# Performance work log

Hardware: AMD Instinct MI355X
Metric: run time of the kernel (lower is better)

Reference implementation:

```python
import jax, jax.numpy as jnp
import numpy as np

B, V, SX, SY, TIN = 4, 3, 256, 256, 10
WIDTH, M1, M2, STEP, VOUT, NL = 32, 16, 16, 10, 3, 6


def setup_inputs() -> dict:
    key = jax.random.key(0)
    ks = jax.random.split(key, 20)
    n = lambda k, s, sc=1.0: sc * jax.random.normal(k, s, dtype=jnp.float32)
    u = lambda k, s: jax.random.uniform(k, s, dtype=jnp.float32)
    sc = 1.0 / WIDTH
    cshape = (NL, WIDTH, WIDTH, V, M1, M2)
    return {
        'x': n(ks[0], (B, V, SX, SY, TIN)),
        'fc0_w': n(ks[1], (TIN + 2, WIDTH), 0.1), 'fc0_b': jnp.zeros((WIDTH,), jnp.float32),
        'w1r': sc * u(ks[2], cshape), 'w1i': sc * u(ks[3], cshape),
        'w2r': sc * u(ks[4], cshape), 'w2i': sc * u(ks[5], cshape),
        'm1w': n(ks[6], (NL, WIDTH, WIDTH), 0.05), 'm1b': jnp.zeros((NL, WIDTH), jnp.float32),
        'm2w': n(ks[7], (NL, WIDTH, WIDTH), 0.05), 'm2b': jnp.zeros((NL, WIDTH), jnp.float32),
        'ww': n(ks[8], (NL, WIDTH, WIDTH), 0.05), 'wb': jnp.zeros((NL, WIDTH), jnp.float32),
        'bw': n(ks[9], (NL, WIDTH, 2), 0.1), 'bb': jnp.zeros((NL, WIDTH), jnp.float32),
        'fc1v_w': n(ks[10], (V, VOUT), 0.3), 'fc1v_b': jnp.zeros((VOUT,), jnp.float32),
        'fc1t_w': n(ks[11], (WIDTH, 256), 0.05), 'fc1t_b': jnp.zeros((256,), jnp.float32),
        'fc2t_w': n(ks[12], (256, STEP), 0.05), 'fc2t_b': jnp.zeros((STEP,), jnp.float32),
    }


def _gelu(t):
    return jax.nn.gelu(t, approximate=False)  # torch F.gelu default = exact erf


def _conv1x1(x, w, b):
    # 1x1x1 Conv3d: channel mix only. x: (b,c,v,x,y), w: (out,in)
    return jnp.einsum('bcvxy,oc->bovxy', x, w) + b[None, :, None, None, None]


def _spectral(x, w1, w2):
    # x: (b,c,v,X,Y); rfft2 over (X,Y); mode-truncated complex mix, zero-pad, irfft2
    sx, sy = x.shape[-2], x.shape[-1]
    xf = jnp.fft.rfft2(x)  # (b,c,v,X,Y//2+1) complex64
    o1 = jnp.einsum('bivxy,iovxy->bovxy', xf[..., :M1, :M2], w1)
    o2 = jnp.einsum('bivxy,iovxy->bovxy', xf[..., -M1:, :M2], w2)
    out = jnp.zeros((x.shape[0], w1.shape[1]) + xf.shape[2:], jnp.complex64)
    out = out.at[..., :M1, :M2].set(o1).at[..., -M1:, :M2].set(o2)
    return jnp.fft.irfft2(out, s=(sx, sy))


def reference(x, fc0_w, fc0_b, w1r, w1i, w2r, w2i, m1w, m1b, m2w, m2b, ww, wb, bw, bb,
              fc1v_w, fc1v_b, fc1t_w, fc1t_b, fc2t_w, fc2t_b):
    b, v, sx, sy, _ = x.shape
    gx = jnp.broadcast_to(jnp.linspace(0.0, 1.0, sx, dtype=jnp.float32)[:, None], (sx, sy))
    gy = jnp.broadcast_to(jnp.linspace(0.0, 1.0, sy, dtype=jnp.float32)[None, :], (sx, sy))
    grid = jnp.broadcast_to(jnp.stack([gx, gy], -1)[None, None], (b, v, sx, sy, 2))
    h = jnp.concatenate([x, grid], -1) @ fc0_w + fc0_b  # (b,v,X,Y,C)
    h = h.transpose(0, 4, 1, 2, 3)  # (b,C,v,X,Y)
    g = grid.transpose(0, 4, 1, 2, 3)  # (b,2,v,X,Y)

    def layer(i, t):
        x1 = _spectral(t, w1r[i] + 1j * w1i[i], w2r[i] + 1j * w2i[i])
        x1 = _conv1x1(_gelu(_conv1x1(x1, m1w[i], m1b[i])), m2w[i], m2b[i])
        x2 = _conv1x1(t, ww[i], wb[i])
        x3 = _conv1x1(g, bw[i], bb[i])
        return _gelu(x1 + x2 + x3)

    h0 = layer(0, h)
    h = layer(1, h0)
    h = layer(2, h) + h0
    h1 = layer(3, h)
    h = layer(4, h1)
    h = layer(5, h) + h1

    h = h.transpose(0, 1, 3, 4, 2)  # (b,C,X,Y,v)
    h = _gelu(h @ fc1v_w + fc1v_b)
    h = h.transpose(0, 4, 2, 3, 1)  # (b,vout,X,Y,C)
    h = _gelu(h @ fc1t_w + fc1t_b)
    return h @ fc2t_w + fc2t_b  # (b,vout,X,Y,step)
```

## Files before the change

kernel.cpp:

```cpp
#include <hip/hip_runtime.h>
#include <math.h>


#define OFF_A   0
#define OFF_B   25165824
#define OFF_T   50331648
#define OFF_XF  53477376
#define OFF_T1  54263808
#define OFF_T2T 54272000
#define OFF_TAC 54288384
#define OFF_TAS 54296576
#define OFF_TB  54304768

__device__ __forceinline__ float geluf(float x) {
    float a = fabsf(x) * 0.70710678118654752f;
    float t = __builtin_amdgcn_rcpf(fmaf(0.3275911f, a, 1.0f));
    float p = t * fmaf(t, fmaf(t, fmaf(t, fmaf(t, 1.061405429f, -1.453152027f),
                                       1.421413741f), -0.284496736f), 0.254829592f);
    float e = __expf(-a * a);
    float erfa = fmaf(-p, e, 1.0f);
    float er = copysignf(erfa, x);
    return 0.5f * x * (1.0f + er);
}

__global__ void k_init_tables(float* __restrict__ ws) {
    const float W0 = 6.2831853071795864769f / 256.0f;
    int stride = gridDim.x * blockDim.x;
    int tid = blockIdx.x * blockDim.x + threadIdx.x;
    for (int i = tid; i < 4096; i += stride) {
        int m = i >> 5, q = i & 31, g = q >> 2, j = q & 3;
        int k0 = 4 * (g & 3) + (g >> 2);
        int k = k0 + 2 * (j >> 1);
        float th = W0 * (float)((k * m) & 255);
        ws[OFF_T1 + i] = (j & 1) ? -sinf(th) : cosf(th);
    }
    for (int idx = tid; idx < 8192; idx += stride) {
        int n = idx >> 5, kx = idx & 31;
        int KX = (kx < 16) ? kx : (kx + 224);
        float th = W0 * (float)((KX * n) & 255);
        ws[OFF_T2T + 2*idx]     = cosf(th);
        ws[OFF_T2T + 2*idx + 1] = sinf(th);
    }
    for (int idx = tid; idx < 8192; idx += stride) {
        int kx = idx >> 8, n = idx & 255;
        int KX = (kx < 16) ? kx : (kx + 224);
        float th = W0 * (float)((KX * n) & 255);
        ws[OFF_TAC + idx] = cosf(th);
        ws[OFF_TAS + idx] = sinf(th);
    }
    for (int idx = tid; idx < 8192; idx += stride) {
        int j = idx >> 8, m = idx & 255, k = j >> 1;
        float th = W0 * (float)((k * m) & 255);
        float beta = (k == 0) ? (1.0f/65536.0f) : (2.0f/65536.0f);
        float val;
        if (j & 1) val = (k == 0) ? 0.0f : -beta * sinf(th);
        else       val = beta * cosf(th);
        ws[OFF_TB + idx] = val;
    }
}

__device__ __forceinline__ void fold_lds(float* lds, int tid) {
#pragma unroll
    for (int it = 0; it < 16; ++it) {
        int pi = it * 256 + tid;
        int r = pi >> 7, mm = pi & 127;
        float* row = lds + r * 257;
        float a = row[mm], c = row[mm + 128];
        row[mm] = a + c; row[mm + 128] = a - c;
    }
}

__device__ __forceinline__ void dft_row_phase(const float* lds, const float* __restrict__ tabF,
                                              float* __restrict__ T, int b, int v, int n, int tid) {
    int r = tid >> 3, g = tid & 7;
    int p = g >> 2, idx = g & 3;
    const float* dp = lds + r * 257 + p * 128;
    const float* tp = tabF + g * 4;
    float a0 = 0.f, a1 = 0.f, a2 = 0.f, a3 = 0.f;
#pragma unroll 4
    for (int m = 0; m < 128; ++m) {
        float d = dp[m];
        float4 t = *(const float4*)(tp + m * 32);
        a0 += d * t.x; a1 += d * t.y; a2 += d * t.z; a3 += d * t.w;
    }
    size_t trow = ((size_t)((b * 32 + r) * 3 + v) * 256 + n) * 32;
    float2 w0; w0.x = a0; w0.y = a1;
    float2 w1; w1.x = a2; w1.y = a3;
    *(float2*)(T + trow + 8 * idx + 2 * p) = w0;
    *(float2*)(T + trow + 8 * idx + 2 * p + 4) = w1;
}

__global__ __launch_bounds__(256) void k_fc0(const float* __restrict__ x,
                                             const float* __restrict__ w,
                                             const float* __restrict__ bias,
                                             float* __restrict__ outA,
                                             float* __restrict__ T,
                                             const float* __restrict__ tabF) {
    __shared__ float lds[32 * 257];
    int blk = blockIdx.x;
    int m = threadIdx.x;
    int n = blk & 255;
    int bv = blk >> 8;
    int v = bv % 3, b = bv / 3;
    const float* xp = x + ((size_t)blk * 256 + m) * 10;
    float xin[10];
#pragma unroll
    for (int t = 0; t < 10; t++) xin[t] = xp[t];
    float gx = (float)n * (1.0f/255.0f), gy = (float)m * (1.0f/255.0f);
    float* op = outA + ((size_t)(b*96) + v) * 65536 + n * 256 + m;
#pragma unroll
    for (int c = 0; c < 32; c++) {
        float a = bias[c] + gx * w[10*32 + c] + gy * w[11*32 + c];
#pragma unroll
        for (int t = 0; t < 10; t++) a += xin[t] * w[t*32 + c];
        op[(size_t)c * 196608] = a;
        lds[c * 257 + m] = a;
    }
    __syncthreads();
    fold_lds(lds, m);
    __syncthreads();
    dft_row_phase(lds, tabF, T, b, v, n, m);
}

__global__ __launch_bounds__(256) void k_dft_x(const float* __restrict__ T,
                                               float* __restrict__ XFp,
                                               const float* __restrict__ tab2) {
    __shared__ float lds[4096];
    int idx = blockIdx.x;
    int half = idx & 1; int blk = idx >> 1;
    int i = blk & 31; int bv = blk >> 5;
    int b = bv / 3, v = bv - 3*b;
    int tid = threadIdx.x;
    const float4* slab = (const float4*)(T + (size_t)((b*32 + i)*3 + v) * 8192 + half * 4096);
#pragma unroll
    for (int j = 0; j < 4; ++j)
        ((float4*)lds)[j * 256 + tid] = slab[j * 256 + tid];
    __syncthreads();
    int ky = tid & 15, kxh = tid >> 4;
    const float* t2b = tab2 + half * 128 * 64;
    float r0=0.f, i0=0.f, r1=0.f, i1=0.f;
#pragma unroll 2
    for (int nn = 0; nn < 128; nn++) {
        float2 t = *(const float2*)(lds + nn * 32 + 2 * ky);
        float2 cs0 = *(const float2*)(t2b + nn*64 + kxh*2);
        float2 cs1 = *(const float2*)(t2b + nn*64 + (kxh+16)*2);
        r0 += t.x*cs0.x + t.y*cs0.y;  i0 += t.y*cs0.x - t.x*cs0.y;
        r1 += t.x*cs1.x + t.y*cs1.y;  i1 += t.y*cs1.x - t.x*cs1.y;
    }
    float2* xfp = (float2*)(XFp + (size_t)(half * 384 + blk) * 1024);
    float2 v0; v0.x = r0; v0.y = i0;
    float2 v1; v1.x = r1; v1.y = i1;
    xfp[kxh*16 + ky] = v0;
    xfp[(kxh+16)*16 + ky] = v1;
}

__global__ __launch_bounds__(256) void k_mixidft(const float* __restrict__ XFp,
                                                 float* __restrict__ T2,
                                                 const float* __restrict__ w1r,
                                                 const float* __restrict__ w1i,
                                                 const float* __restrict__ w2r,
                                                 const float* __restrict__ w2i,
                                                 const float* __restrict__ tac,
                                                 const float* __restrict__ tas, int l) {
    __shared__ float Olds[2048];
    int idx = blockIdx.x;
    int half = idx & 1; int blk = idx >> 1;
    int o = blk & 31; int bv = blk >> 5;
    int b = bv / 3, v = bv - 3*b;
    int tid = threadIdx.x;
    {
        int ky = tid & 15, kxh = tid >> 4;
        float R0=0.f, I0=0.f, R1=0.f, I1=0.f;
#pragma unroll
        for (int i = 0; i < 32; i++) {
            const float2* xa = (const float2*)(XFp + (size_t)(bv*32 + i) * 1024);
            const float2* xb = (const float2*)(XFp + (size_t)(384 + bv*32 + i) * 1024);
            float2 p0 = xa[kxh*16 + ky], q0 = xb[kxh*16 + ky];
            float2 p1 = xa[(kxh+16)*16 + ky], q1 = xb[(kxh+16)*16 + ky];
            float2 xf0; xf0.x = p0.x + q0.x; xf0.y = p0.y + q0.y;
            float2 xf1; xf1.x = p1.x + q1.x; xf1.y = p1.y + q1.y;
            size_t wbase = ((size_t)((l*32 + i)*32 + o)*3 + v) * 256;
            float a1r = w1r[wbase + tid], a1i = w1i[wbase + tid];
            float a2r = w2r[wbase + tid], a2i = w2i[wbase + tid];
            R0 += xf0.x*a1r - xf0.y*a1i;  I0 += xf0.x*a1i + xf0.y*a1r;
            R1 += xf1.x*a2r - xf1.y*a2i;  I1 += xf1.x*a2i + xf1.y*a2r;
        }
        float2 v0; v0.x = R0; v0.y = I0;
        float2 v1; v1.x = R1; v1.y = I1;
        ((float2*)Olds)[kxh*16 + ky] = v0;
        ((float2*)Olds)[(kxh+16)*16 + ky] = v1;
    }
    __syncthreads();
    {
        int ky2 = tid & 31, n8 = tid >> 5;
        int ky = ky2 >> 1, ri = ky2 & 1;
        float* t2p = T2 + (size_t)((b*32 + o)*3 + v) * 8192;
#pragma unroll 2
        for (int ii = 0; ii < 16; ++ii) {
            int n = half * 128 + ii*8 + n8;
            float acc = 0.f;
#pragma unroll
            for (int kx = 0; kx < 32; ++kx) {
                float2 ov = ((const float2*)Olds)[kx*16 + ky];
                float c = tac[kx*256 + n], s = tas[kx*256 + n];
                float ca = ri ? s : c;
                float cb = ri ? c : -s;
                acc += ov.x*ca + ov.y*cb;
            }
            t2p[n*32 + ky2] = acc;
        }
    }
}

template<int HAS_SKIP, int DO_DFT>
__global__ __launch_bounds__(256) void k_conv(
    const float* IN, float* OUT, const float* SK,
    const float* __restrict__ T2, const float* __restrict__ tabB,
    const float* __restrict__ m1w, const float* __restrict__ m1b,
    const float* __restrict__ m2w, const float* __restrict__ m2b,
    const float* __restrict__ ww,  const float* __restrict__ wb,
    const float* __restrict__ bw,  const float* __restrict__ bb,
    float* __restrict__ Tout, const float* __restrict__ tabF, int l)
{
    __shared__ float t2s[1024];
    __shared__ float lds[DO_DFT ? 32 * 257 : 1];
    int blk = blockIdx.x;
    int m = threadIdx.x;
    int n = blk & 255; int bv = blk >> 8;
    int b = bv / 3, v = bv - 3*b;

    {
        int c = m >> 3, q = m & 7;
        const float4* src = (const float4*)(T2 + (size_t)b * 786432 + (size_t)c * 24576
                                            + v * 8192 + n * 32 + q * 4);
        ((float4*)t2s)[m] = *src;
    }
    float tb[32];
#pragma unroll
    for (int j = 0; j < 32; j++) tb[j] = tabB[j*256 + m];
    __syncthreads();

    const float* inp = IN + (size_t)(b*96 + v) * 65536 + n * 256 + m;
    float hv[32];
#pragma unroll
    for (int c = 0; c < 32; c++) hv[c] = inp[(size_t)c * 196608];

    float x1[32];
#pragma unroll
    for (int c = 0; c < 32; c++) {
        const float4* q = (const float4*)(t2s + c*32);
        float a = 0.f;
#pragma unroll
        for (int jj = 0; jj < 8; jj++) {
            float4 qv = q[jj];
            a = fmaf(qv.x, tb[jj*4+0], a);
            a = fmaf(qv.y, tb[jj*4+1], a);
            a = fmaf(qv.z, tb[jj*4+2], a);
            a = fmaf(qv.w, tb[jj*4+3], a);
        }
        x1[c] = a;
    }

    const float* m1wl = m1w + l*1024; const float* m1bl = m1b + l*32;
    float g1[32];
#pragma unroll
    for (int o = 0; o < 32; o++) {
        float a = m1bl[o];
#pragma unroll
        for (int c = 0; c < 32; c++) a = fmaf(m1wl[o*32 + c], x1[c], a);
        g1[o] = geluf(a);
    }

    const float* m2wl = m2w + l*1024; const float* m2bl = m2b + l*32;
    const float* wwl  = ww  + l*1024; const float* wbl  = wb  + l*32;
    const float* bwl  = bw  + l*64;   const float* bbl  = bb  + l*32;
    float gx = (float)n * (1.0f/255.0f), gy = (float)m * (1.0f/255.0f);
    float* outp = OUT + (size_t)(b*96 + v) * 65536 + n * 256 + m;
    const float* skp = SK + (size_t)(b*96 + v) * 65536 + n * 256 + m;

#pragma unroll
    for (int o = 0; o < 32; o++) {
        float a = m2bl[o] + wbl[o] + bbl[o] + bwl[o*2]*gx + bwl[o*2+1]*gy;
#pragma unroll
        for (int c = 0; c < 32; c++) a = fmaf(m2wl[o*32 + c], g1[c], a);
#pragma unroll
        for (int c = 0; c < 32; c++) a = fmaf(wwl[o*32 + c], hv[c], a);
        float val = geluf(a);
        if (HAS_SKIP) val += skp[(size_t)o * 196608];
        outp[(size_t)o * 196608] = val;
        if (DO_DFT) lds[o * 257 + m] = val;
    }
    if (DO_DFT) {
        __syncthreads();
        fold_lds(lds, m);
        __syncthreads();
        dft_row_phase(lds, tabF, Tout, b, v, n, m);
    }
}

__global__ __launch_bounds__(256) void k_final(
    const float* __restrict__ IN, float* __restrict__ OUT,
    const float* __restrict__ w1v, const float* __restrict__ b1v,
    const float* __restrict__ w1t, const float* __restrict__ b1t,
    const float* __restrict__ w2t, const float* __restrict__ b2t)
{
    int blk = blockIdx.x;
    int m = threadIdx.x;
    int vo = blk % 3; int rest = blk / 3;
    int n = rest & 255, b = rest >> 8;
    const float* inp = IN + (size_t)(b*96) * 65536 + n * 256 + m;

    float wv0 = w1v[vo], wv1 = w1v[3 + vo], wv2 = w1v[6 + vo], bv0 = b1v[vo];
    float Av[32];
#pragma unroll
    for (int c = 0; c < 32; c++) {
        float f0 = inp[(size_t)(c*3 + 0) * 65536];
        float f1 = inp[(size_t)(c*3 + 1) * 65536];
        float f2 = inp[(size_t)(c*3 + 2) * 65536];
        Av[c] = geluf(f0*wv0 + f1*wv1 + f2*wv2 + bv0);
    }

    float acc[10];
#pragma unroll
    for (int s = 0; s < 10; s++) acc[s] = 0.f;

#pragma unroll 4
    for (int u = 0; u < 256; u++) {
        float t = b1t[u];
#pragma unroll
        for (int c = 0; c < 32; c++) t = fmaf(Av[c], w1t[c*256 + u], t);
        t = geluf(t);
#pragma unroll
        for (int s = 0; s < 10; s++) acc[s] = fmaf(t, w2t[u*10 + s], acc[s]);
    }

    float* outp = OUT + ((size_t)(b*3 + vo) * 65536 + (size_t)(n * 256 + m)) * 10;
#pragma unroll
    for (int s = 0; s < 10; s++) outp[s] = acc[s] + b2t[s];
}

extern "C" void kernel_launch(void* const* d_in, const int* in_sizes, int n_in,
                              void* d_out, int out_size, void* d_ws, size_t ws_size,
                              hipStream_t stream) {
    const float* x    = (const float*)d_in[0];
    const float* fc0w = (const float*)d_in[1];
    const float* fc0b = (const float*)d_in[2];
    const float* w1r  = (const float*)d_in[3];
    const float* w1i  = (const float*)d_in[4];
    const float* w2r  = (const float*)d_in[5];
    const float* w2i  = (const float*)d_in[6];
    const float* m1w  = (const float*)d_in[7];
    const float* m1b  = (const float*)d_in[8];
    const float* m2w  = (const float*)d_in[9];
    const float* m2b  = (const float*)d_in[10];
    const float* ww   = (const float*)d_in[11];
    const float* wb   = (const float*)d_in[12];
    const float* bw   = (const float*)d_in[13];
    const float* bb   = (const float*)d_in[14];
    const float* w1v  = (const float*)d_in[15];
    const float* b1v  = (const float*)d_in[16];
    const float* w1t  = (const float*)d_in[17];
    const float* b1t  = (const float*)d_in[18];
    const float* w2t  = (const float*)d_in[19];
    const float* b2t  = (const float*)d_in[20];

    float* ws   = (float*)d_ws;
    float* A    = ws + OFF_A;
    float* Bu   = ws + OFF_B;
    float* T    = ws + OFF_T;
    float* XFp  = ws + OFF_XF;
    float* tabF = ws + OFF_T1;
    float* tab2 = ws + OFF_T2T;
    float* tac  = ws + OFF_TAC;
    float* tas  = ws + OFF_TAS;
    float* tbB  = ws + OFF_TB;

    k_init_tables<<<64, 256, 0, stream>>>(ws);
    k_fc0<<<3072, 256, 0, stream>>>(x, fc0w, fc0b, A, T, tabF);

    float* lin [6] = {A, A, Bu, Bu, A, Bu};
    float* lout[6] = {A, Bu, Bu, A, Bu, Bu};
    const float* lskip[6] = {nullptr, nullptr, A, nullptr, nullptr, A};

    for (int l = 0; l < 6; l++) {
        k_dft_x<<<768, 256, 0, stream>>>(T, XFp, tab2);
        k_mixidft<<<768, 256, 0, stream>>>(XFp, T, w1r, w1i, w2r, w2i, tac, tas, l);
        int skip = lskip[l] != nullptr, dodft = (l < 5);
        if (skip && dodft)
            k_conv<1,1><<<3072, 256, 0, stream>>>(lin[l], lout[l], lskip[l], T, tbB,
                                                  m1w, m1b, m2w, m2b, ww, wb, bw, bb, T, tabF, l);
        else if (!skip && dodft)
            k_conv<0,1><<<3072, 256, 0, stream>>>(lin[l], lout[l], nullptr, T, tbB,
                                                  m1w, m1b, m2w, m2b, ww, wb, bw, bb, T, tabF, l);
        else if (skip && !dodft)
            k_conv<1,0><<<3072, 256, 0, stream>>>(lin[l], lout[l], lskip[l], T, tbB,
                                                  m1w, m1b, m2w, m2b, ww, wb, bw, bb, T, tabF, l);
        else
            k_conv<0,0><<<3072, 256, 0, stream>>>(lin[l], lout[l], nullptr, T, tbB,
                                                  m1w, m1b, m2w, m2b, ww, wb, bw, bb, T, tabF, l);
    }

    k_final<<<3072, 256, 0, stream>>>(Bu, (float*)d_out, w1v, b1v, w1t, b1t, w2t, b2t);
}
```

Baseline: 2.367 ms.

## Fold m1 channel mix into spectral weights and split DFT over eight parts

Uses linearity of the inverse DFT to fold the first 1x1 conv weights (m1w) into the complex spectral weights with a new per-layer k_foldw kernel. This removes the 32x32 x1 mixing loop from each pixel in k_conv. The x-direction DFT and mixidft are also split into 8 partial-sum parts (3072 blocks) instead of 2, for more parallelism, at the cost of summing 8 partials per input channel. Scratch for the folded weights and partials is placed in the output buffer before k_final overwrites it, which adds a per-layer fold kernel and extra partial-sum traffic.

```diff
diff --git a/kernel.cpp b/kernel.cpp
--- a/kernel.cpp
+++ b/kernel.cpp
@@ -5,12 +5,14 @@
 #define OFF_A   0
 #define OFF_B   25165824
 #define OFF_T   50331648
-#define OFF_XF  53477376
 #define OFF_T1  54263808
 #define OFF_T2T 54272000
 #define OFF_TAC 54288384
 #define OFF_TAS 54296576
 #define OFF_TB  54304768
+
+#define DO_FW   0
+#define DO_XF   3145728
 
 __device__ __forceinline__ float geluf(float x) {
     float a = fabsf(x) * 0.70710678118654752f;
@@ -56,6 +58,34 @@
         if (j & 1) val = (k == 0) ? 0.0f : -beta * sinf(th);
         else       val = beta * cosf(th);
         ws[OFF_TB + idx] = val;
+    }
+}
+
+__global__ __launch_bounds__(256) void k_foldw(const float* __restrict__ w1r_l,
+                                               const float* __restrict__ w1i_l,
+                                               const float* __restrict__ w2r_l,
+                                               const float* __restrict__ w2i_l,
+                                               const float* __restrict__ m1w_l,
+                                               float2* __restrict__ fp1,
+                                               float2* __restrict__ fp2) {
+    int blk = blockIdx.x;
+    int p = threadIdx.x;
+    int op = blk & 31; int i = blk >> 5;
+    const float* mrow = m1w_l + op*32;
+#pragma unroll
+    for (int v = 0; v < 3; ++v) {
+        float a1r = 0.f, a1i = 0.f, a2r = 0.f, a2i = 0.f;
+#pragma unroll 4
+        for (int o = 0; o < 32; ++o) {
+            float mw = mrow[o];
+            size_t idx = ((size_t)(i*32 + o)*3 + v)*256 + p;
+            a1r = fmaf(mw, w1r_l[idx], a1r); a1i = fmaf(mw, w1i_l[idx], a1i);
+            a2r = fmaf(mw, w2r_l[idx], a2r); a2i = fmaf(mw, w2i_l[idx], a2i);
+        }
+        size_t oidx = ((size_t)(i*32 + op)*3 + v)*256 + p;
+        float2 u1; u1.x = a1r; u1.y = a1i;
+        float2 u2; u2.x = a2r; u2.y = a2i;
+        fp1[oidx] = u1; fp2[oidx] = u2;
     }
 }
 
@@ -125,29 +155,27 @@
 __global__ __launch_bounds__(256) void k_dft_x(const float* __restrict__ T,
                                                float* __restrict__ XFp,
                                                const float* __restrict__ tab2) {
-    __shared__ float lds[4096];
+    __shared__ float lds[1024];
     int idx = blockIdx.x;
-    int half = idx & 1; int blk = idx >> 1;
+    int part = idx & 7; int blk = idx >> 3;
     int i = blk & 31; int bv = blk >> 5;
     int b = bv / 3, v = bv - 3*b;
     int tid = threadIdx.x;
-    const float4* slab = (const float4*)(T + (size_t)((b*32 + i)*3 + v) * 8192 + half * 4096);
-#pragma unroll
-    for (int j = 0; j < 4; ++j)
-        ((float4*)lds)[j * 256 + tid] = slab[j * 256 + tid];
+    const float4* slab = (const float4*)(T + (size_t)((b*32 + i)*3 + v) * 8192 + part * 1024);
+    ((float4*)lds)[tid] = slab[tid];
     __syncthreads();
     int ky = tid & 15, kxh = tid >> 4;
-    const float* t2b = tab2 + half * 128 * 64;
+    const float* t2b = tab2 + part * 2048;
     float r0=0.f, i0=0.f, r1=0.f, i1=0.f;
 #pragma unroll 2
-    for (int nn = 0; nn < 128; nn++) {
+    for (int nn = 0; nn < 32; nn++) {
         float2 t = *(const float2*)(lds + nn * 32 + 2 * ky);
         float2 cs0 = *(const float2*)(t2b + nn*64 + kxh*2);
         float2 cs1 = *(const float2*)(t2b + nn*64 + (kxh+16)*2);
         r0 += t.x*cs0.x + t.y*cs0.y;  i0 += t.y*cs0.x - t.x*cs0.y;
         r1 += t.x*cs1.x + t.y*cs1.y;  i1 += t.y*cs1.x - t.x*cs1.y;
     }
-    float2* xfp = (float2*)(XFp + (size_t)(half * 384 + blk) * 1024);
+    float2* xfp = (float2*)(XFp + (size_t)(part * 384 + blk) * 1024);
     float2 v0; v0.x = r0; v0.y = i0;
     float2 v1; v1.x = r1; v1.y = i1;
     xfp[kxh*16 + ky] = v0;
@@ -156,34 +184,35 @@
 
 __global__ __launch_bounds__(256) void k_mixidft(const float* __restrict__ XFp,
                                                  float* __restrict__ T2,
-                                                 const float* __restrict__ w1r,
-                                                 const float* __restrict__ w1i,
-                                                 const float* __restrict__ w2r,
-                                                 const float* __restrict__ w2i,
+                                                 const float2* __restrict__ fp1,
+                                                 const float2* __restrict__ fp2,
                                                  const float* __restrict__ tac,
-                                                 const float* __restrict__ tas, int l) {
+                                                 const float* __restrict__ tas) {
     __shared__ float Olds[2048];
     int idx = blockIdx.x;
-    int half = idx & 1; int blk = idx >> 1;
+    int part = idx & 7; int blk = idx >> 3;
     int o = blk & 31; int bv = blk >> 5;
     int b = bv / 3, v = bv - 3*b;
     int tid = threadIdx.x;
     {
         int ky = tid & 15, kxh = tid >> 4;
         float R0=0.f, I0=0.f, R1=0.f, I1=0.f;
-#pragma unroll
+#pragma unroll 4
         for (int i = 0; i < 32; i++) {
-            const float2* xa = (const float2*)(XFp + (size_t)(bv*32 + i) * 1024);
-            const float2* xb = (const float2*)(XFp + (size_t)(384 + bv*32 + i) * 1024);
-            float2 p0 = xa[kxh*16 + ky], q0 = xb[kxh*16 + ky];
-            float2 p1 = xa[(kxh+16)*16 + ky], q1 = xb[(kxh+16)*16 + ky];
-            float2 xf0; xf0.x = p0.x + q0.x; xf0.y = p0.y + q0.y;
-            float2 xf1; xf1.x = p1.x + q1.x; xf1.y = p1.y + q1.y;
-            size_t wbase = ((size_t)((l*32 + i)*32 + o)*3 + v) * 256;
-            float a1r = w1r[wbase + tid], a1i = w1i[wbase + tid];
-            float a2r = w2r[wbase + tid], a2i = w2i[wbase + tid];
-            R0 += xf0.x*a1r - xf0.y*a1i;  I0 += xf0.x*a1i + xf0.y*a1r;
-            R1 += xf1.x*a2r - xf1.y*a2i;  I1 += xf1.x*a2i + xf1.y*a2r;
+            size_t xbase = (size_t)(bv*32 + i) * 1024;
+            float x0r=0.f, x0i=0.f, x1r=0.f, x1i=0.f;
+#pragma unroll
+            for (int p = 0; p < 8; p++) {
+                const float2* xp = (const float2*)(XFp + (size_t)(p * 384) * 1024 + xbase);
+                float2 a = xp[kxh*16 + ky];
+                float2 c = xp[(kxh+16)*16 + ky];
+                x0r += a.x; x0i += a.y; x1r += c.x; x1i += c.y;
+            }
+            size_t wbase = ((size_t)(i*32 + o)*3 + v) * 256;
+            float2 u1 = fp1[wbase + tid];
+            float2 u2 = fp2[wbase + tid];
+            R0 += x0r*u1.x - x0i*u1.y;  I0 += x0r*u1.y + x0i*u1.x;
+            R1 += x1r*u2.x - x1i*u2.y;  I1 += x1r*u2.y + x1i*u2.x;
         }
         float2 v0; v0.x = R0; v0.y = I0;
         float2 v1; v1.x = R1; v1.y = I1;
@@ -195,9 +224,9 @@
         int ky2 = tid & 31, n8 = tid >> 5;
         int ky = ky2 >> 1, ri = ky2 & 1;
         float* t2p = T2 + (size_t)((b*32 + o)*3 + v) * 8192;
-#pragma unroll 2
-        for (int ii = 0; ii < 16; ++ii) {
-            int n = half * 128 + ii*8 + n8;
+#pragma unroll
+        for (int ii = 0; ii < 4; ++ii) {
+            int n = part*32 + ii*8 + n8;
             float acc = 0.f;
 #pragma unroll
             for (int kx = 0; kx < 32; ++kx) {
@@ -216,7 +245,7 @@
 __global__ __launch_bounds__(256) void k_conv(
     const float* IN, float* OUT, const float* SK,
     const float* __restrict__ T2, const float* __restrict__ tabB,
-    const float* __restrict__ m1w, const float* __restrict__ m1b,
+    const float* __restrict__ m1b,
     const float* __restrict__ m2w, const float* __restrict__ m2b,
     const float* __restrict__ ww,  const float* __restrict__ wb,
     const float* __restrict__ bw,  const float* __restrict__ bb,
@@ -245,11 +274,12 @@
 #pragma unroll
     for (int c = 0; c < 32; c++) hv[c] = inp[(size_t)c * 196608];
 
-    float x1[32];
-#pragma unroll
-    for (int c = 0; c < 32; c++) {
-        const float4* q = (const float4*)(t2s + c*32);
-        float a = 0.f;
+    const float* m1bl = m1b + l*32;
+    float g1[32];
+#pragma unroll
+    for (int o = 0; o < 32; o++) {
+        const float4* q = (const float4*)(t2s + o*32);
+        float a = m1bl[o];
 #pragma unroll
         for (int jj = 0; jj < 8; jj++) {
             float4 qv = q[jj];
@@ -258,16 +288,6 @@
             a = fmaf(qv.z, tb[jj*4+2], a);
             a = fmaf(qv.w, tb[jj*4+3], a);
         }
-        x1[c] = a;
-    }
-
-    const float* m1wl = m1w + l*1024; const float* m1bl = m1b + l*32;
-    float g1[32];
-#pragma unroll
-    for (int o = 0; o < 32; o++) {
-        float a = m1bl[o];
-#pragma unroll
-        for (int c = 0; c < 32; c++) a = fmaf(m1wl[o*32 + c], x1[c], a);
         g1[o] = geluf(a);
     }
 
@@ -368,13 +388,17 @@
     float* A    = ws + OFF_A;
     float* Bu   = ws + OFF_B;
     float* T    = ws + OFF_T;
-    float* XFp  = ws + OFF_XF;
     float* tabF = ws + OFF_T1;
     float* tab2 = ws + OFF_T2T;
     float* tac  = ws + OFF_TAC;
     float* tas  = ws + OFF_TAS;
     float* tbB  = ws + OFF_TB;
 
+    float* dout = (float*)d_out;
+    float2* fp1 = (float2*)(dout + DO_FW);
+    float2* fp2 = (float2*)(dout + DO_FW + 1572864);
+    float* XFp  = dout + DO_XF;
+
     k_init_tables<<<64, 256, 0, stream>>>(ws);
     k_fc0<<<3072, 256, 0, stream>>>(x, fc0w, fc0b, A, T, tabF);
 
@@ -383,21 +407,24 @@
     const float* lskip[6] = {nullptr, nullptr, A, nullptr, nullptr, A};
 
     for (int l = 0; l < 6; l++) {
-        k_dft_x<<<768, 256, 0, stream>>>(T, XFp, tab2);
-        k_mixidft<<<768, 256, 0, stream>>>(XFp, T, w1r, w1i, w2r, w2i, tac, tas, l);
+        k_foldw<<<1024, 256, 0, stream>>>(w1r + (size_t)l*786432, w1i + (size_t)l*786432,
+                                          w2r + (size_t)l*786432, w2i + (size_t)l*786432,
+                                          m1w + l*1024, fp1, fp2);
+        k_dft_x<<<3072, 256, 0, stream>>>(T, XFp, tab2);
+        k_mixidft<<<3072, 256, 0, stream>>>(XFp, T, fp1, fp2, tac, tas);
         int skip = lskip[l] != nullptr, dodft = (l < 5);
         if (skip && dodft)
             k_conv<1,1><<<3072, 256, 0, stream>>>(lin[l], lout[l], lskip[l], T, tbB,
-                                                  m1w, m1b, m2w, m2b, ww, wb, bw, bb, T, tabF, l);
+                                                  m1b, m2w, m2b, ww, wb, bw, bb, T, tabF, l);
         else if (!skip && dodft)
             k_conv<0,1><<<3072, 256, 0, stream>>>(lin[l], lout[l], nullptr, T, tbB,
-                                                  m1w, m1b, m2w, m2b, ww, wb, bw, bb, T, tabF, l);
+                                                  m1b, m2w, m2b, ww, wb, bw, bb, T, tabF, l);
         else if (skip && !dodft)
             k_conv<1,0><<<3072, 256, 0, stream>>>(lin[l], lout[l], lskip[l], T, tbB,
-                                                  m1w, m1b, m2w, m2b, ww, wb, bw, bb, T, tabF, l);
+                                                  m1b, m2w, m2b, ww, wb, bw, bb, T, tabF, l);
         else
             k_conv<0,0><<<3072, 256, 0, stream>>>(lin[l], lout[l], nullptr, T, tbB,
-                                                  m1w, m1b, m2w, m2b, ww, wb, bw, bb, T, tabF, l);
+                                                  m1b, m2w, m2b, ww, wb, bw, bb, T, tabF, l);
     }
 
     k_final<<<3072, 256, 0, stream>>>(Bu, (float*)d_out, w1v, b1v, w1t, b1t, w2t, b2t);
```

Result: slower. 3.126 ms (+32.1%).
